# Kernel optimization log

Measured on AMD Instinct MI355X. Metric: run time of the kernel, lower is better.

The kernel has to match this reference:

```python
import jax, jax.numpy as jnp
import numpy as np

N = 50000      # nodes
E = 800000     # edges (avg degree 16)
D_IN = 64
H = 128        # capacity
LAT = 64       # latent_dim
LN_EPS = 1e-5


def setup_inputs() -> dict:
    key = jax.random.key(0)
    ks = jax.random.split(key, 16)
    inp = {}
    inp["x"] = jax.random.normal(ks[0], (N, D_IN), dtype=jnp.float32)
    inp["edge_index"] = jax.random.randint(ks[1], (2, E), 0, N)
    dims = [(D_IN, H), (H, H), (H, LAT)]
    ki = 2
    for t in ("m", "v"):  # mu tower / logvar tower
        for i, (di, do) in enumerate(dims):
            s = 1.0 / np.sqrt(di)
            inp[f"{t}Wl{i}"] = jax.random.normal(ks[ki], (do, di), jnp.float32) * s; ki += 1
            inp[f"{t}bl{i}"] = jnp.zeros((do,), jnp.float32)
            inp[f"{t}Wr{i}"] = jax.random.normal(ks[ki], (do, di), jnp.float32) * s; ki += 1
            if i < 2:  # LayerNorm on hidden layers only
                inp[f"{t}g{i}"] = jnp.ones((do,), jnp.float32)
                inp[f"{t}b{i}"] = jnp.zeros((do,), jnp.float32)
    return inp


def _ln(h, g, b):
    m = h.mean(-1, keepdims=True)
    v = h.var(-1, keepdims=True)
    return (h - m) * jax.lax.rsqrt(v + LN_EPS) * g + b


def _sage(h, src, dst, inv_deg, Wl, bl, Wr):
    # mean neighbor aggregation: scatter-add messages h[src] into dst, divide by degree
    agg = jax.ops.segment_sum(h[src], dst, num_segments=N) * inv_deg  # [N, d_in]
    # PyG SAGEConv: lin_l(agg) [with bias] + lin_r(h_root) [no bias]
    return agg @ Wl.T + bl + h @ Wr.T


def _tower(x, src, dst, inv_deg, layers):
    h = x
    L = len(layers)
    for i, lay in enumerate(layers):
        h = _sage(h, src, dst, inv_deg, lay[0], lay[1], lay[2])
        if i < L - 1:
            h = jax.nn.relu(_ln(h, lay[3], lay[4]))
    return h


def reference(x, edge_index,
              mWl0, mbl0, mWr0, mg0, mb0,
              mWl1, mbl1, mWr1, mg1, mb1,
              mWl2, mbl2, mWr2,
              vWl0, vbl0, vWr0, vg0, vb0,
              vWl1, vbl1, vWr1, vg1, vb1,
              vWl2, vbl2, vWr2):
    src, dst = edge_index[0], edge_index[1]
    deg = jax.ops.segment_sum(jnp.ones((E,), x.dtype), dst, num_segments=N)
    inv_deg = (1.0 / jnp.maximum(deg, 1.0))[:, None]
    mu_layers = [(mWl0, mbl0, mWr0, mg0, mb0),
                 (mWl1, mbl1, mWr1, mg1, mb1),
                 (mWl2, mbl2, mWr2)]
    lv_layers = [(vWl0, vbl0, vWr0, vg0, vb0),
                 (vWl1, vbl1, vWr1, vg1, vb1),
                 (vWl2, vbl2, vWr2)]
    mu = _tower(x, src, dst, inv_deg, mu_layers)
    lv = _tower(x, src, dst, inv_deg, lv_layers)
    return mu, lv
```

## Files before the change

### kernel.cpp

```cpp
#include <hip/hip_runtime.h>

#define NN 50000
#define NE 800000
#define MPAD 50048
#define NBK 196
#define FB 98
#define CH4 2048
#define EB4 200000
#define STAGE_CAP 6144

typedef __attribute__((ext_vector_type(8))) short short8;
typedef __attribute__((ext_vector_type(4))) float f32x4;

__device__ __forceinline__ ushort f2b(float f) {
    uint u = __builtin_bit_cast(uint, f);
    uint r = (u + 0x7fffu + ((u >> 16) & 1u)) >> 16;
    return (ushort)r;
}
__device__ __forceinline__ uint pk2(float a, float b) {
    return (uint)f2b(a) | ((uint)f2b(b) << 16);
}
__device__ __forceinline__ float blo(uint u) { return __builtin_bit_cast(float, u << 16); }
__device__ __forceinline__ float bhi(uint u) { return __builtin_bit_cast(float, u & 0xffff0000u); }

__global__ __launch_bounds__(256) void k_f1(const int* __restrict__ dst, int* __restrict__ bhist) {
    __shared__ int h[NBK];
    for (int i = threadIdx.x; i < NBK; i += 256) h[i] = 0;
    __syncthreads();
    int i1 = min((int)(blockIdx.x + 1) * CH4, EB4);
    for (int i = blockIdx.x * CH4 + threadIdx.x; i < i1; i += 256) {
        int4 d = ((const int4*)dst)[i];
        atomicAdd(&h[d.x >> 8], 1);
        atomicAdd(&h[d.y >> 8], 1);
        atomicAdd(&h[d.z >> 8], 1);
        atomicAdd(&h[d.w >> 8], 1);
    }
    __syncthreads();
    for (int i = threadIdx.x; i < NBK; i += 256) bhist[blockIdx.x * NBK + i] = h[i];
}

__global__ __launch_bounds__(256) void k_fscan(const int* __restrict__ bhist,
                                               int* __restrict__ pairRel,
                                               int* __restrict__ bbase) {
    __shared__ int tot[256];
    int b = threadIdx.x;
    int run = 0;
    if (b < NBK) {
        for (int blk = 0; blk < FB; ++blk) {
            int v = bhist[blk * NBK + b];
            pairRel[blk * NBK + b] = run;
            run += v;
        }
    }
    tot[b] = (b < NBK) ? run : 0;
    __syncthreads();
    for (int off = 1; off < 256; off <<= 1) {
        int t = (b >= off) ? tot[b - off] : 0;
        __syncthreads();
        tot[b] += t;
        __syncthreads();
    }
    if (b < NBK) bbase[b] = tot[b] - run;
    if (b == NBK - 1) bbase[NBK] = tot[b];
}

__global__ __launch_bounds__(256) void k_f2(const int* __restrict__ src, const int* __restrict__ dst,
                                            const int* __restrict__ pairRel,
                                            const int* __restrict__ bbase, int2* __restrict__ pairs) {
    __shared__ int cur[NBK];
    for (int i = threadIdx.x; i < NBK; i += 256)
        cur[i] = bbase[i] + pairRel[blockIdx.x * NBK + i];
    __syncthreads();
    int i1 = min((int)(blockIdx.x + 1) * CH4, EB4);
    for (int i = blockIdx.x * CH4 + threadIdx.x; i < i1; i += 256) {
        int4 s = ((const int4*)src)[i];
        int4 d = ((const int4*)dst)[i];
        int p0 = atomicAdd(&cur[d.x >> 8], 1);
        int p1 = atomicAdd(&cur[d.y >> 8], 1);
        int p2 = atomicAdd(&cur[d.z >> 8], 1);
        int p3 = atomicAdd(&cur[d.w >> 8], 1);
        pairs[p0] = (int2){s.x, d.x};
        pairs[p1] = (int2){s.y, d.y};
        pairs[p2] = (int2){s.z, d.z};
        pairs[p3] = (int2){s.w, d.w};
    }
}

__global__ __launch_bounds__(256) void k_f3(const int2* __restrict__ pairs,
                                            const int* __restrict__ bbase,
                                            int* __restrict__ row_start,
                                            float* __restrict__ inv_deg,
                                            int* __restrict__ col) {
    __shared__ int ndeg[256];
    __shared__ int noff[256];
    __shared__ int stage[STAGE_CAP];
    int b = blockIdx.x;
    int base = bbase[b], end = bbase[b + 1];
    int nbase = b << 8;
    int t = threadIdx.x;
    ndeg[t] = 0;
    __syncthreads();
    for (int p = base + t; p < end; p += 256) atomicAdd(&ndeg[pairs[p].y - nbase], 1);
    __syncthreads();
    int d = ndeg[t];
    noff[t] = d;
    __syncthreads();
    for (int off = 1; off < 256; off <<= 1) {
        int v = (t >= off) ? noff[t - off] : 0;
        __syncthreads();
        noff[t] += v;
        __syncthreads();
    }
    int excl = noff[t] - d;
    int node = nbase + t;
    if (node < NN) {
        row_start[node] = base + excl;
        inv_deg[node] = 1.0f / (float)(d > 1 ? d : 1);
    }
    if (b == 0 && t == 0) row_start[NN] = NE;
    __syncthreads();
    noff[t] = excl;
    __syncthreads();
    int cnt = end - base;
    for (int p = base + t; p < end; p += 256) {
        int2 pr = pairs[p];
        int pos = atomicAdd(&noff[pr.y - nbase], 1);
        if (pos < STAGE_CAP) stage[pos] = pr.x;
        else col[base + pos] = pr.x;
    }
    __syncthreads();
    int lim = cnt < STAGE_CAP ? cnt : STAGE_CAP;
    for (int i = t; i < lim; i += 256) col[base + i] = stage[i];
}


__global__ void k_xcvt(const float* __restrict__ x, ushort* __restrict__ xb, int n2) {
    int i = blockIdx.x * blockDim.x + threadIdx.x;
    if (i < n2) {
        float2 v = *(const float2*)(x + (size_t)i * 2);
        *(uint*)(xb + (size_t)i * 2) = pk2(v.x, v.y);
    }
}

struct W2Args {
    const float* srcA[8];
    const float* srcB[8];
    ushort* dst[8];
};

__global__ void k_wcvt(W2Args a) {
    const int offT[8]   = {0, 16384, 49152, 57344, 65536, 81920, 114688, 122880};
    const int splitT[8] = {64, 128, 128, 0, 64, 128, 128, 0};
    const int logKKT[8] = {7, 8, 7, 7, 7, 8, 7, 7};
    const int ntT[8]    = {8, 8, 4, 4, 8, 8, 4, 4};
    int idx = blockIdx.x * blockDim.x + threadIdx.x;
    if (idx >= 131072) return;
    int L = 0;
#pragma unroll
    for (int i = 1; i < 8; ++i) if (idx >= offT[i]) L = i;
    int j = idx - offT[L];
    int lk = logKKT[L];
    int KK = 1 << lk;
    int n = j >> lk;
    int c = j & (KK - 1);
    int split = splitT[L];
    float v = (c < split) ? a.srcA[L][n * split + c]
                          : a.srcB[L][n * (KK - split) + (c - split)];
    int ks = c >> 5, kseg = (c >> 3) & 3, jj = c & 7;
    int nt = n >> 4, r15 = n & 15;
    int lane = (kseg << 4) | r15;
    int foff = ((ks * ntT[L] + nt) << 9) + (lane << 3) + jj;
    a.dst[L][foff] = f2b(v);
}


__device__ __forceinline__ void acc8(float* a, uint4 u) {
    a[0] += blo(u.x); a[1] += bhi(u.x);
    a[2] += blo(u.y); a[3] += bhi(u.y);
    a[4] += blo(u.z); a[5] += bhi(u.z);
    a[6] += blo(u.w); a[7] += bhi(u.w);
}
__device__ __forceinline__ void acc4(float* a, uint2 u) {
    a[0] += blo(u.x); a[1] += bhi(u.x);
    a[2] += blo(u.y); a[3] += bhi(u.y);
}

template <int D>
__global__ __launch_bounds__(256) void k_agg(
    const ushort* __restrict__ h,
    const int* __restrict__ row_start, const int* __restrict__ col,
    const float* __restrict__ inv_deg, ushort* __restrict__ o) {
    int node = (blockIdx.x * 256 + threadIdx.x) >> 4;
    int li = threadIdx.x & 15;
    if (node >= NN) return;
    int s = row_start[node], e = row_start[node + 1];
    float sc = inv_deg[node];
    if (D == 128) {
        const ushort* hb = h + (size_t)li * 8;
        float a[8] = {0, 0, 0, 0, 0, 0, 0, 0};
        int p = s;
        for (; p + 7 < e; p += 8) {
            int c0 = col[p], c1 = col[p + 1], c2 = col[p + 2], c3 = col[p + 3];
            int c4 = col[p + 4], c5 = col[p + 5], c6 = col[p + 6], c7 = col[p + 7];
            uint4 u0 = *(const uint4*)(hb + (size_t)c0 * 128);
            uint4 u1 = *(const uint4*)(hb + (size_t)c1 * 128);
            uint4 u2 = *(const uint4*)(hb + (size_t)c2 * 128);
            uint4 u3 = *(const uint4*)(hb + (size_t)c3 * 128);
            uint4 u4 = *(const uint4*)(hb + (size_t)c4 * 128);
            uint4 u5 = *(const uint4*)(hb + (size_t)c5 * 128);
            uint4 u6 = *(const uint4*)(hb + (size_t)c6 * 128);
            uint4 u7 = *(const uint4*)(hb + (size_t)c7 * 128);
            acc8(a, u0); acc8(a, u1); acc8(a, u2); acc8(a, u3);
            acc8(a, u4); acc8(a, u5); acc8(a, u6); acc8(a, u7);
        }
        for (; p < e; ++p) acc8(a, *(const uint4*)(hb + (size_t)col[p] * 128));
        uint4 r;
        r.x = pk2(a[0] * sc, a[1] * sc);
        r.y = pk2(a[2] * sc, a[3] * sc);
        r.z = pk2(a[4] * sc, a[5] * sc);
        r.w = pk2(a[6] * sc, a[7] * sc);
        *(uint4*)(o + (size_t)node * 128 + li * 8) = r;
    } else {
        const ushort* hb = h + (size_t)li * 4;
        float a[4] = {0, 0, 0, 0};
        int p = s;
        for (; p + 7 < e; p += 8) {
            int c0 = col[p], c1 = col[p + 1], c2 = col[p + 2], c3 = col[p + 3];
            int c4 = col[p + 4], c5 = col[p + 5], c6 = col[p + 6], c7 = col[p + 7];
            uint2 u0 = *(const uint2*)(hb + (size_t)c0 * 64);
            uint2 u1 = *(const uint2*)(hb + (size_t)c1 * 64);
            uint2 u2 = *(const uint2*)(hb + (size_t)c2 * 64);
            uint2 u3 = *(const uint2*)(hb + (size_t)c3 * 64);
            uint2 u4 = *(const uint2*)(hb + (size_t)c4 * 64);
            uint2 u5 = *(const uint2*)(hb + (size_t)c5 * 64);
            uint2 u6 = *(const uint2*)(hb + (size_t)c6 * 64);
            uint2 u7 = *(const uint2*)(hb + (size_t)c7 * 64);
            acc4(a, u0); acc4(a, u1); acc4(a, u2); acc4(a, u3);
            acc4(a, u4); acc4(a, u5); acc4(a, u6); acc4(a, u7);
        }
        for (; p < e; ++p) acc4(a, *(const uint2*)(hb + (size_t)col[p] * 64));
        uint2 r;
        r.x = pk2(a[0] * sc, a[1] * sc);
        r.y = pk2(a[2] * sc, a[3] * sc);
        *(uint2*)(o + (size_t)node * 64 + li * 4) = r;
    }
}

__global__ __launch_bounds__(256) void k_agg256(
    const ushort* __restrict__ h,
    const int* __restrict__ row_start, const int* __restrict__ col,
    const float* __restrict__ inv_deg, ushort* __restrict__ o) {
    int node = (blockIdx.x * 256 + threadIdx.x) >> 5;
    int li = threadIdx.x & 31;
    if (node >= NN) return;
    int s = row_start[node], e = row_start[node + 1];
    float sc = inv_deg[node];
    const ushort* hb = h + (size_t)li * 8;
    float a[8] = {0, 0, 0, 0, 0, 0, 0, 0};
    int p = s;
    for (; p + 7 < e; p += 8) {
        int c0 = col[p], c1 = col[p + 1], c2 = col[p + 2], c3 = col[p + 3];
        int c4 = col[p + 4], c5 = col[p + 5], c6 = col[p + 6], c7 = col[p + 7];
        uint4 u0 = *(const uint4*)(hb + (size_t)c0 * 256);
        uint4 u1 = *(const uint4*)(hb + (size_t)c1 * 256);
        uint4 u2 = *(const uint4*)(hb + (size_t)c2 * 256);
        uint4 u3 = *(const uint4*)(hb + (size_t)c3 * 256);
        uint4 u4 = *(const uint4*)(hb + (size_t)c4 * 256);
        uint4 u5 = *(const uint4*)(hb + (size_t)c5 * 256);
        uint4 u6 = *(const uint4*)(hb + (size_t)c6 * 256);
        uint4 u7 = *(const uint4*)(hb + (size_t)c7 * 256);
        acc8(a, u0); acc8(a, u1); acc8(a, u2); acc8(a, u3);
        acc8(a, u4); acc8(a, u5); acc8(a, u6); acc8(a, u7);
    }
    for (; p < e; ++p) acc8(a, *(const uint4*)(hb + (size_t)col[p] * 256));
    uint4 r;
    r.x = pk2(a[0] * sc, a[1] * sc);
    r.y = pk2(a[2] * sc, a[3] * sc);
    r.z = pk2(a[4] * sc, a[5] * sc);
    r.w = pk2(a[6] * sc, a[7] * sc);
    *(uint4*)(o + (size_t)node * 256 + li * 8) = r;
}


struct GArgs {
    const ushort *A1, *A2, *Wm, *Wv;
    const float *blm, *blv, *gm, *gv, *bbm, *bbv;
    void* out;
};

template <int KH, int NOUT, bool DO_LN, bool DUAL, int ASTR, int AOFFM, int OSTR, int OOFFM>
__global__ __launch_bounds__(256, 2) void k_gemm(GArgs a) {
    constexpr int NT = NOUT / 16;
    constexpr int NK = KH / 16;
    constexpr int TW = DUAL ? 2 : 1;
    constexpr int WCH = NOUT * KH * 4 / 16;
    __shared__ uint4 wlds[TW * WCH];

    int tid = threadIdx.x;
    int lane = tid & 63, wid = tid >> 6;
    int tow = DUAL ? 0 : blockIdx.y;
    int aoff = tow * AOFFM;

    {
        const uint4* w0 = (const uint4*)(tow ? a.Wv : a.Wm);
        for (int i = tid; i < WCH; i += 256) wlds[i] = w0[i];
        if (DUAL) {
            const uint4* w1 = (const uint4*)a.Wv;
            for (int i = tid; i < WCH; i += 256) wlds[WCH + i] = w1[i];
        }
    }

    int r15 = lane & 15, kseg = lane >> 4;
    int m0 = blockIdx.x * 128 + wid * 32;
    size_t ar0 = (size_t)(m0 + r15);
    size_t ar1 = (size_t)(m0 + 16 + r15);

    short8 af[2][NK];
#pragma unroll
    for (int ks = 0; ks < NK; ++ks) {
        int kc = ks * 32 + kseg * 8;
        af[0][ks] = (kc < KH) ? *(const short8*)(a.A1 + ar0 * ASTR + aoff + kc)
                              : *(const short8*)(a.A2 + ar0 * ASTR + aoff + (kc - KH));
        af[1][ks] = (kc < KH) ? *(const short8*)(a.A1 + ar1 * ASTR + aoff + kc)
                              : *(const short8*)(a.A2 + ar1 * ASTR + aoff + (kc - KH));
    }
    __syncthreads();

    f32x4 acc[TW][2][NT];
#pragma unroll
    for (int tt = 0; tt < TW; ++tt)
#pragma unroll
        for (int t = 0; t < 2; ++t)
#pragma unroll
            for (int nt = 0; nt < NT; ++nt) acc[tt][t][nt] = (f32x4){0.f, 0.f, 0.f, 0.f};

#pragma unroll
    for (int ks = 0; ks < NK; ++ks) {
#pragma unroll
        for (int nt = 0; nt < NT; ++nt) {
#pragma unroll
            for (int tt = 0; tt < TW; ++tt) {
                short8 w = *(const short8*)&wlds[tt * WCH + (ks * NT + nt) * 64 + lane];
                acc[tt][0][nt] = __builtin_amdgcn_mfma_f32_16x16x32_bf16(af[0][ks], w, acc[tt][0][nt], 0, 0, 0);
                acc[tt][1][nt] = __builtin_amdgcn_mfma_f32_16x16x32_bf16(af[1][ks], w, acc[tt][1][nt], 0, 0, 0);
            }
        }
    }

#pragma unroll
    for (int tt = 0; tt < TW; ++tt) {
        int tsel = DUAL ? tt : tow;
        int ooff = tsel * OOFFM;
        const float* bl = tsel ? a.blv : a.blm;
#pragma unroll
        for (int nt = 0; nt < NT; ++nt) {
            float bb = bl[nt * 16 + r15];
#pragma unroll
            for (int t = 0; t < 2; ++t)
#pragma unroll
                for (int r = 0; r < 4; ++r) acc[tt][t][nt][r] += bb;
        }
        if (DO_LN) {
            const float* g = tsel ? a.gv : a.gm;
            const float* b = tsel ? a.bbv : a.bbm;
#pragma unroll
            for (int t = 0; t < 2; ++t) {
                float s[4] = {0, 0, 0, 0}, q[4] = {0, 0, 0, 0};
#pragma unroll
                for (int nt = 0; nt < NT; ++nt)
#pragma unroll
                    for (int r = 0; r < 4; ++r) { float v = acc[tt][t][nt][r]; s[r] += v; q[r] += v * v; }
#pragma unroll
                for (int off = 1; off < 16; off <<= 1)
#pragma unroll
                    for (int r = 0; r < 4; ++r) { s[r] += __shfl_xor(s[r], off); q[r] += __shfl_xor(q[r], off); }
                float mean[4], rstd[4];
#pragma unroll
                for (int r = 0; r < 4; ++r) {
                    mean[r] = s[r] * (1.0f / NOUT);
                    float var = q[r] * (1.0f / NOUT) - mean[r] * mean[r];
                    rstd[r] = rsqrtf(var + 1e-5f);
                }
                ushort* out = (ushort*)a.out;
#pragma unroll
                for (int nt = 0; nt < NT; ++nt) {
                    int n = nt * 16 + r15;
                    float gg = g[n], bb = b[n];
#pragma unroll
                    for (int r = 0; r < 4; ++r) {
                        int row = m0 + t * 16 + kseg * 4 + r;
                        if (row < NN) {
                            float y = fmaxf((acc[tt][t][nt][r] - mean[r]) * rstd[r] * gg + bb, 0.0f);
                            out[(size_t)row * OSTR + ooff + n] = f2b(y);
                        }
                    }
                }
            }
        } else {
            float* out = (float*)a.out;
#pragma unroll
            for (int t = 0; t < 2; ++t)
#pragma unroll
                for (int nt = 0; nt < NT; ++nt) {
                    int n = nt * 16 + r15;
#pragma unroll
                    for (int r = 0; r < 4; ++r) {
                        int row = m0 + t * 16 + kseg * 4 + r;
                        if (row < NN) out[(size_t)row * OSTR + ooff + n] = acc[tt][t][nt][r];
                    }
                }
        }
    }
}


struct G2Args {
    const ushort *A, *Wm, *Wv, *a2;
    const float *blm, *blv;
    void *outm, *outv;
};

template <bool FINAL>
__global__ __launch_bounds__(256, 2) void k_gemm2(G2Args a) {
    constexpr int NT = 4, NK = 4;
    constexpr int WCH = 1024;
    __shared__ uint4 wlds[WCH];

    int tid = threadIdx.x;
    int lane = tid & 63, wid = tid >> 6;
    int tow = blockIdx.y;
    {
        const uint4* w0 = (const uint4*)(tow ? a.Wv : a.Wm);
        for (int i = tid; i < WCH; i += 256) wlds[i] = w0[i];
    }
    int r15 = lane & 15, kseg = lane >> 4;
    int m0 = blockIdx.x * 128 + wid * 32;
    size_t ar0 = (size_t)(m0 + r15);
    size_t ar1 = (size_t)(m0 + 16 + r15);
    int aoff = tow * 128;

    short8 af[2][NK];
#pragma unroll
    for (int ks = 0; ks < NK; ++ks) {
        int kc = ks * 32 + kseg * 8;
        af[0][ks] = *(const short8*)(a.A + ar0 * 256 + aoff + kc);
        af[1][ks] = *(const short8*)(a.A + ar1 * 256 + aoff + kc);
    }
    __syncthreads();

    f32x4 acc[2][NT];
#pragma unroll
    for (int t = 0; t < 2; ++t)
#pragma unroll
        for (int nt = 0; nt < NT; ++nt) acc[t][nt] = (f32x4){0.f, 0.f, 0.f, 0.f};

#pragma unroll
    for (int ks = 0; ks < NK; ++ks) {
#pragma unroll
        for (int nt = 0; nt < NT; ++nt) {
            short8 w = *(const short8*)&wlds[(ks * NT + nt) * 64 + lane];
            acc[0][nt] = __builtin_amdgcn_mfma_f32_16x16x32_bf16(af[0][ks], w, acc[0][nt], 0, 0, 0);
            acc[1][nt] = __builtin_amdgcn_mfma_f32_16x16x32_bf16(af[1][ks], w, acc[1][nt], 0, 0, 0);
        }
    }

    if (FINAL) {
        const float* bl = tow ? a.blv : a.blm;
        float* out = (float*)(tow ? a.outv : a.outm);
#pragma unroll
        for (int t = 0; t < 2; ++t)
#pragma unroll
            for (int nt = 0; nt < NT; ++nt) {
                int n = nt * 16 + r15;
                float bb = bl[n];
#pragma unroll
                for (int r = 0; r < 4; ++r) {
                    int row = m0 + t * 16 + kseg * 4 + r;
                    if (row < NN) {
                        float av = blo((uint)a.a2[(size_t)row * 128 + tow * 64 + n]);
                        out[(size_t)row * 64 + n] = acc[t][nt][r] + bb + av;
                    }
                }
            }
    } else {
        ushort* out = (ushort*)a.outm;
#pragma unroll
        for (int t = 0; t < 2; ++t)
#pragma unroll
            for (int nt = 0; nt < NT; ++nt) {
                int n = nt * 16 + r15;
#pragma unroll
                for (int r = 0; r < 4; ++r) {
                    int row = m0 + t * 16 + kseg * 4 + r;
                    if (row < NN) out[(size_t)row * 128 + tow * 64 + n] = f2b(acc[t][nt][r]);
                }
            }
    }
}


extern "C" void kernel_launch(void* const* d_in, const int* in_sizes, int n_in,
                              void* d_out, int out_size, void* d_ws, size_t ws_size,
                              hipStream_t stream) {
    const float* x = (const float*)d_in[0];
    const int* ei = (const int*)d_in[1];
    const int* esrc = ei;
    const int* edst = ei + NE;

    const float* mWl0 = (const float*)d_in[2];
    const float* mbl0 = (const float*)d_in[3];
    const float* mWr0 = (const float*)d_in[4];
    const float* mg0  = (const float*)d_in[5];
    const float* mb0  = (const float*)d_in[6];
    const float* mWl1 = (const float*)d_in[7];
    const float* mbl1 = (const float*)d_in[8];
    const float* mWr1 = (const float*)d_in[9];
    const float* mg1  = (const float*)d_in[10];
    const float* mb1  = (const float*)d_in[11];
    const float* mWl2 = (const float*)d_in[12];
    const float* mbl2 = (const float*)d_in[13];
    const float* mWr2 = (const float*)d_in[14];
    const float* vWl0 = (const float*)d_in[15];
    const float* vbl0 = (const float*)d_in[16];
    const float* vWr0 = (const float*)d_in[17];
    const float* vg0  = (const float*)d_in[18];
    const float* vb0  = (const float*)d_in[19];
    const float* vWl1 = (const float*)d_in[20];
    const float* vbl1 = (const float*)d_in[21];
    const float* vWr1 = (const float*)d_in[22];
    const float* vg1  = (const float*)d_in[23];
    const float* vb1  = (const float*)d_in[24];
    const float* vWl2 = (const float*)d_in[25];
    const float* vbl2 = (const float*)d_in[26];
    const float* vWr2 = (const float*)d_in[27];

    char* p = (char*)d_ws;
    auto alloc = [&](size_t bytes) {
        void* r = (void*)p;
        p += (bytes + 255) & ~(size_t)255;
        return r;
    };
    int* bhist     = (int*)alloc((size_t)FB * NBK * 4);
    int* pairRel   = (int*)alloc((size_t)FB * NBK * 4);
    int* bbase     = (int*)alloc((size_t)(NBK + 1) * 4);
    int* row_start = (int*)alloc((size_t)(NN + 1) * 4);
    float* inv_deg = (float*)alloc((size_t)NN * 4);
    int* col       = (int*)alloc((size_t)NE * 4);
    int2* pairs    = (int2*)alloc((size_t)NE * 8);
    ushort* agg0   = (ushort*)pairs;
    ushort* x_bf   = (ushort*)alloc((size_t)MPAD * 64 * 2);
    ushort* h1p    = (ushort*)alloc((size_t)MPAD * 256 * 2);
    ushort* h2p    = (ushort*)alloc((size_t)MPAD * 256 * 2);
    ushort* aggp   = (ushort*)alloc((size_t)MPAD * 256 * 2);
    ushort* p2     = aggp;
    ushort* a2     = aggp + (size_t)MPAD * 128;
    ushort* wc0    = (ushort*)alloc((size_t)128 * 128 * 2);
    ushort* wc1    = (ushort*)alloc((size_t)128 * 256 * 2);
    ushort* wc2    = (ushort*)alloc((size_t)64 * 128 * 2);
    ushort* wc3    = (ushort*)alloc((size_t)128 * 128 * 2);
    ushort* wc4    = (ushort*)alloc((size_t)128 * 256 * 2);
    ushort* wc5    = (ushort*)alloc((size_t)64 * 128 * 2);
    ushort* wc6    = (ushort*)alloc((size_t)64 * 128 * 2);
    ushort* wc7    = (ushort*)alloc((size_t)64 * 128 * 2);

    float* out_mu = (float*)d_out;
    float* out_lv = (float*)d_out + (size_t)NN * 64;

    k_xcvt<<<(NN * 64 / 2 + 255) / 256, 256, 0, stream>>>(x, x_bf, NN * 64 / 2);
    W2Args wa;
    wa.srcA[0] = mWl0; wa.srcB[0] = mWr0; wa.dst[0] = wc0;
    wa.srcA[1] = mWl1; wa.srcB[1] = mWr1; wa.dst[1] = wc1;
    wa.srcA[2] = mWl2; wa.srcB[2] = nullptr; wa.dst[2] = wc2;
    wa.srcA[3] = nullptr; wa.srcB[3] = mWr2; wa.dst[3] = wc6;
    wa.srcA[4] = vWl0; wa.srcB[4] = vWr0; wa.dst[4] = wc3;
    wa.srcA[5] = vWl1; wa.srcB[5] = vWr1; wa.dst[5] = wc4;
    wa.srcA[6] = vWl2; wa.srcB[6] = nullptr; wa.dst[6] = wc5;
    wa.srcA[7] = nullptr; wa.srcB[7] = vWr2; wa.dst[7] = wc7;
    k_wcvt<<<512, 256, 0, stream>>>(wa);

    k_f1<<<FB, 256, 0, stream>>>(edst, bhist);
    k_fscan<<<1, 256, 0, stream>>>(bhist, pairRel, bbase);
    k_f2<<<FB, 256, 0, stream>>>(esrc, edst, pairRel, bbase, pairs);
    k_f3<<<196, 256, 0, stream>>>(pairs, bbase, row_start, inv_deg, col);

    const int gA16 = (NN * 16 + 255) / 256;
    const int gA32 = (NN * 32 + 255) / 256;
    const int gM = MPAD / 128;

    k_agg<64><<<gA16, 256, 0, stream>>>(x_bf, row_start, col, inv_deg, agg0);
    {
        GArgs ga = {agg0, x_bf, wc0, wc3, mbl0, vbl0, mg0, vg0, mb0, vb0, h1p};
        k_gemm<64, 128, true, true, 64, 0, 256, 128><<<dim3(gM, 1), 256, 0, stream>>>(ga);
    }
    k_agg256<<<gA32, 256, 0, stream>>>(h1p, row_start, col, inv_deg, aggp);
    {
        GArgs ga = {aggp, h1p, wc1, wc4, mbl1, vbl1, mg1, vg1, mb1, vb1, h2p};
        k_gemm<128, 128, true, false, 256, 128, 256, 128><<<dim3(gM, 2), 256, 0, stream>>>(ga);
    }
    {
        G2Args g2 = {h2p, wc2, wc5, nullptr, nullptr, nullptr, p2, nullptr};
        k_gemm2<false><<<dim3(gM, 2), 256, 0, stream>>>(g2);
    }
    k_agg<128><<<gA16, 256, 0, stream>>>(p2, row_start, col, inv_deg, a2);
    {
        G2Args g2 = {h2p, wc6, wc7, a2, mbl2, vbl2, out_mu, out_lv};
        k_gemm2<true><<<dim3(gM, 2), 256, 0, stream>>>(g2);
    }
}
```

Measured before the change: 359.0 us.

## Slice feature columns across blocks in neighbor aggregation for cache locality

Replaces the three aggregation kernels with one templated kernel that splits each node's feature row into 32-column slices, one slice per block. Each block handles 64 nodes, with 4 lanes per node covering 32 bf16 columns using 16-byte loads. The intent is to shrink the working set each gather touches at a time (64-byte segments per row) so the scattered neighbor reads hit L2/MALL more often. The cost is that col indices and row_start are re-read once per slice, and the number of blocks grows by the slice count.

New measurement: 392.7 us. 9.4% more time.

```diff
diff --git a/kernel.cpp b/kernel.cpp
--- a/kernel.cpp
+++ b/kernel.cpp
@@ -22,6 +22,7 @@
 }
 __device__ __forceinline__ float blo(uint u) { return __builtin_bit_cast(float, u << 16); }
 __device__ __forceinline__ float bhi(uint u) { return __builtin_bit_cast(float, u & 0xffff0000u); }
+
 
 __global__ __launch_bounds__(256) void k_f1(const int* __restrict__ dst, int* __restrict__ bhist) {
     __shared__ int h[NBK];
@@ -180,105 +181,43 @@
     a[4] += blo(u.z); a[5] += bhi(u.z);
     a[6] += blo(u.w); a[7] += bhi(u.w);
 }
-__device__ __forceinline__ void acc4(float* a, uint2 u) {
-    a[0] += blo(u.x); a[1] += bhi(u.x);
-    a[2] += blo(u.y); a[3] += bhi(u.y);
-}
-
-template <int D>
-__global__ __launch_bounds__(256) void k_agg(
+
+template <int D, int NSLICE>
+__global__ __launch_bounds__(256) void k_aggs(
     const ushort* __restrict__ h,
     const int* __restrict__ row_start, const int* __restrict__ col,
     const float* __restrict__ inv_deg, ushort* __restrict__ o) {
-    int node = (blockIdx.x * 256 + threadIdx.x) >> 4;
-    int li = threadIdx.x & 15;
+    int slice = blockIdx.x % NSLICE;
+    int chunk = blockIdx.x / NSLICE;
+    int node = chunk * 64 + (threadIdx.x >> 2);
+    int li = threadIdx.x & 3;
     if (node >= NN) return;
     int s = row_start[node], e = row_start[node + 1];
     float sc = inv_deg[node];
-    if (D == 128) {
-        const ushort* hb = h + (size_t)li * 8;
-        float a[8] = {0, 0, 0, 0, 0, 0, 0, 0};
-        int p = s;
-        for (; p + 7 < e; p += 8) {
-            int c0 = col[p], c1 = col[p + 1], c2 = col[p + 2], c3 = col[p + 3];
-            int c4 = col[p + 4], c5 = col[p + 5], c6 = col[p + 6], c7 = col[p + 7];
-            uint4 u0 = *(const uint4*)(hb + (size_t)c0 * 128);
-            uint4 u1 = *(const uint4*)(hb + (size_t)c1 * 128);
-            uint4 u2 = *(const uint4*)(hb + (size_t)c2 * 128);
-            uint4 u3 = *(const uint4*)(hb + (size_t)c3 * 128);
-            uint4 u4 = *(const uint4*)(hb + (size_t)c4 * 128);
-            uint4 u5 = *(const uint4*)(hb + (size_t)c5 * 128);
-            uint4 u6 = *(const uint4*)(hb + (size_t)c6 * 128);
-            uint4 u7 = *(const uint4*)(hb + (size_t)c7 * 128);
-            acc8(a, u0); acc8(a, u1); acc8(a, u2); acc8(a, u3);
-            acc8(a, u4); acc8(a, u5); acc8(a, u6); acc8(a, u7);
-        }
-        for (; p < e; ++p) acc8(a, *(const uint4*)(hb + (size_t)col[p] * 128));
-        uint4 r;
-        r.x = pk2(a[0] * sc, a[1] * sc);
-        r.y = pk2(a[2] * sc, a[3] * sc);
-        r.z = pk2(a[4] * sc, a[5] * sc);
-        r.w = pk2(a[6] * sc, a[7] * sc);
-        *(uint4*)(o + (size_t)node * 128 + li * 8) = r;
-    } else {
-        const ushort* hb = h + (size_t)li * 4;
-        float a[4] = {0, 0, 0, 0};
-        int p = s;
-        for (; p + 7 < e; p += 8) {
-            int c0 = col[p], c1 = col[p + 1], c2 = col[p + 2], c3 = col[p + 3];
-            int c4 = col[p + 4], c5 = col[p + 5], c6 = col[p + 6], c7 = col[p + 7];
-            uint2 u0 = *(const uint2*)(hb + (size_t)c0 * 64);
-            uint2 u1 = *(const uint2*)(hb + (size_t)c1 * 64);
-            uint2 u2 = *(const uint2*)(hb + (size_t)c2 * 64);
-            uint2 u3 = *(const uint2*)(hb + (size_t)c3 * 64);
-            uint2 u4 = *(const uint2*)(hb + (size_t)c4 * 64);
-            uint2 u5 = *(const uint2*)(hb + (size_t)c5 * 64);
-            uint2 u6 = *(const uint2*)(hb + (size_t)c6 * 64);
-            uint2 u7 = *(const uint2*)(hb + (size_t)c7 * 64);
-            acc4(a, u0); acc4(a, u1); acc4(a, u2); acc4(a, u3);
-            acc4(a, u4); acc4(a, u5); acc4(a, u6); acc4(a, u7);
-        }
-        for (; p < e; ++p) acc4(a, *(const uint2*)(hb + (size_t)col[p] * 64));
-        uint2 r;
-        r.x = pk2(a[0] * sc, a[1] * sc);
-        r.y = pk2(a[2] * sc, a[3] * sc);
-        *(uint2*)(o + (size_t)node * 64 + li * 4) = r;
-    }
-}
-
-__global__ __launch_bounds__(256) void k_agg256(
-    const ushort* __restrict__ h,
-    const int* __restrict__ row_start, const int* __restrict__ col,
-    const float* __restrict__ inv_deg, ushort* __restrict__ o) {
-    int node = (blockIdx.x * 256 + threadIdx.x) >> 5;
-    int li = threadIdx.x & 31;
-    if (node >= NN) return;
-    int s = row_start[node], e = row_start[node + 1];
-    float sc = inv_deg[node];
-    const ushort* hb = h + (size_t)li * 8;
+    const ushort* hb = h + (size_t)slice * 32 + (size_t)li * 8;
     float a[8] = {0, 0, 0, 0, 0, 0, 0, 0};
     int p = s;
     for (; p + 7 < e; p += 8) {
         int c0 = col[p], c1 = col[p + 1], c2 = col[p + 2], c3 = col[p + 3];
         int c4 = col[p + 4], c5 = col[p + 5], c6 = col[p + 6], c7 = col[p + 7];
-        uint4 u0 = *(const uint4*)(hb + (size_t)c0 * 256);
-        uint4 u1 = *(const uint4*)(hb + (size_t)c1 * 256);
-        uint4 u2 = *(const uint4*)(hb + (size_t)c2 * 256);
-        uint4 u3 = *(const uint4*)(hb + (size_t)c3 * 256);
-        uint4 u4 = *(const uint4*)(hb + (size_t)c4 * 256);
-        uint4 u5 = *(const uint4*)(hb + (size_t)c5 * 256);
-        uint4 u6 = *(const uint4*)(hb + (size_t)c6 * 256);
-        uint4 u7 = *(const uint4*)(hb + (size_t)c7 * 256);
+        uint4 u0 = *(const uint4*)(hb + (size_t)c0 * D);
+        uint4 u1 = *(const uint4*)(hb + (size_t)c1 * D);
+        uint4 u2 = *(const uint4*)(hb + (size_t)c2 * D);
+        uint4 u3 = *(const uint4*)(hb + (size_t)c3 * D);
+        uint4 u4 = *(const uint4*)(hb + (size_t)c4 * D);
+        uint4 u5 = *(const uint4*)(hb + (size_t)c5 * D);
+        uint4 u6 = *(const uint4*)(hb + (size_t)c6 * D);
+        uint4 u7 = *(const uint4*)(hb + (size_t)c7 * D);
         acc8(a, u0); acc8(a, u1); acc8(a, u2); acc8(a, u3);
         acc8(a, u4); acc8(a, u5); acc8(a, u6); acc8(a, u7);
     }
-    for (; p < e; ++p) acc8(a, *(const uint4*)(hb + (size_t)col[p] * 256));
+    for (; p < e; ++p) acc8(a, *(const uint4*)(hb + (size_t)col[p] * D));
     uint4 r;
     r.x = pk2(a[0] * sc, a[1] * sc);
     r.y = pk2(a[2] * sc, a[3] * sc);
     r.z = pk2(a[4] * sc, a[5] * sc);
     r.w = pk2(a[6] * sc, a[7] * sc);
-    *(uint4*)(o + (size_t)node * 256 + li * 8) = r;
+    *(uint4*)(o + (size_t)node * D + slice * 32 + li * 8) = r;
 }
 
 
@@ -583,16 +522,15 @@
     k_f2<<<FB, 256, 0, stream>>>(esrc, edst, pairRel, bbase, pairs);
     k_f3<<<196, 256, 0, stream>>>(pairs, bbase, row_start, inv_deg, col);
 
-    const int gA16 = (NN * 16 + 255) / 256;
-    const int gA32 = (NN * 32 + 255) / 256;
+    const int CHK = (NN + 63) / 64;
     const int gM = MPAD / 128;
 
-    k_agg<64><<<gA16, 256, 0, stream>>>(x_bf, row_start, col, inv_deg, agg0);
+    k_aggs<64, 2><<<2 * CHK, 256, 0, stream>>>(x_bf, row_start, col, inv_deg, agg0);
     {
         GArgs ga = {agg0, x_bf, wc0, wc3, mbl0, vbl0, mg0, vg0, mb0, vb0, h1p};
         k_gemm<64, 128, true, true, 64, 0, 256, 128><<<dim3(gM, 1), 256, 0, stream>>>(ga);
     }
-    k_agg256<<<gA32, 256, 0, stream>>>(h1p, row_start, col, inv_deg, aggp);
+    k_aggs<256, 8><<<8 * CHK, 256, 0, stream>>>(h1p, row_start, col, inv_deg, aggp);
     {
         GArgs ga = {aggp, h1p, wc1, wc4, mbl1, vbl1, mg1, vg1, mb1, vb1, h2p};
         k_gemm<128, 128, true, false, 256, 128, 256, 128><<<dim3(gM, 2), 256, 0, stream>>>(ga);
@@ -601,7 +539,7 @@
         G2Args g2 = {h2p, wc2, wc5, nullptr, nullptr, nullptr, p2, nullptr};
         k_gemm2<false><<<dim3(gM, 2), 256, 0, stream>>>(g2);
     }
-    k_agg<128><<<gA16, 256, 0, stream>>>(p2, row_start, col, inv_deg, a2);
+    k_aggs<128, 4><<<4 * CHK, 256, 0, stream>>>(p2, row_start, col, inv_deg, a2);
     {
         G2Args g2 = {h2p, wc6, wc7, a2, mbl2, vbl2, out_mu, out_lv};
         k_gemm2<true><<<dim3(gM, 2), 256, 0, stream>>>(g2);
```
